# Kernel optimization log

Hardware: AMD Instinct MI355X
Metric: run time of the kernel (lower is better)

## Reference

```python
import jax, jax.numpy as jnp
import numpy as np

N_WORDS_BATCH = 16384   # words in the forward batch
EMB_DIM = 128
NUM_ROOTS = 2048
VOCAB = 65536
BOOST = 1.5             # attention_boost_factor
EPS = 1e-8


def setup_inputs() -> dict:
    key = jax.random.key(0)
    k0, k1, k2, k3, k4 = jax.random.split(key, 5)
    word_indices = jax.random.randint(k0, (N_WORDS_BATCH,), 0, VOCAB, dtype=jnp.int32)
    root_map = jax.random.randint(k1, (VOCAB,), 0, NUM_ROOTS, dtype=jnp.int32)
    attention_weights = jax.random.uniform(k2, (N_WORDS_BATCH,), dtype=jnp.float32)
    # kaiming_uniform-like init scale
    root_embeddings = jax.random.normal(k3, (NUM_ROOTS, EMB_DIM), dtype=jnp.float32) / np.sqrt(EMB_DIM).astype(np.float32)
    morpho_transforms = jax.random.normal(k4, (NUM_ROOTS, EMB_DIM, EMB_DIM), dtype=jnp.float32) / np.sqrt(EMB_DIM).astype(np.float32)
    root_bias = jnp.zeros((NUM_ROOTS, EMB_DIM), dtype=jnp.float32)
    return {
        'root_embeddings': root_embeddings,
        'morpho_transforms': morpho_transforms,
        'root_bias': root_bias,
        'attention_weights': attention_weights,
        'word_indices': word_indices,
        'root_map': root_map,
    }


def reference(root_embeddings, morpho_transforms, root_bias, attention_weights, word_indices, root_map):
    num_roots = root_embeddings.shape[0]
    roots = root_map[word_indices]                      # (N,) extract_roots

    # extract_equivariant_features: root-indexed gather + per-root matvec
    embs = root_embeddings[roots]                       # (N, D)
    mats = morpho_transforms[roots]                     # (N, D, D)
    feats = jnp.einsum('nij,nj->ni', mats, embs) + root_bias[roots]

    # compute_root_invariant: segment mean over same-root words, gathered back
    ones = jnp.ones(roots.shape, feats.dtype)
    counts = jax.ops.segment_sum(ones, roots, num_segments=num_roots)      # (R,)
    sums = jax.ops.segment_sum(feats, roots, num_segments=num_roots)       # (R, D)
    inv = (sums / jnp.maximum(counts, 1.0)[:, None])[roots]                # (N, D)

    # boost_attention: weight i is multiplied by BOOST once per other word sharing its root,
    # i.e. w_i * BOOST**(count[root_i] - 1), then softmax(log(w + eps)) over the batch.
    c = counts[roots] - 1.0
    boosted = attention_weights * jnp.power(jnp.float32(BOOST), c)
    boosted = jax.nn.softmax(jnp.log(boosted + EPS))

    return inv * boosted[:, None]
```

## Files before the change

kernel.cpp:

```cpp
#include <hip/hip_runtime.h>

#define N_WORDS 16384
#define EMB 128
#define NROOTS 2048
#define EPS 1e-8f
#define LOG2_BOOST 0.5849625007211562f


__global__ void k_roots_hist(const int* __restrict__ wi, const int* __restrict__ rmap,
                             int* __restrict__ roots, int* __restrict__ counts) {
    int n = blockIdx.x * blockDim.x + threadIdx.x;
    int r = rmap[wi[n]];
    roots[n] = r;
    atomicAdd(&counts[r], 1);
}

__global__ void k_matvec(const float* __restrict__ M, const float* __restrict__ e,
                         const float* __restrict__ b, float* __restrict__ g) {
    int r   = blockIdx.x >> 5;
    int row = ((blockIdx.x & 31) << 2) + (threadIdx.x >> 6);
    int lane = threadIdx.x & 63;
    const float2* mrow = (const float2*)(M + ((size_t)r * EMB + row) * EMB);
    const float2* ev   = (const float2*)(e + (size_t)r * EMB);
    float2 m  = mrow[lane];
    float2 ee = ev[lane];
    float acc = m.x * ee.x + m.y * ee.y;
#pragma unroll
    for (int off = 32; off; off >>= 1) acc += __shfl_xor(acc, off, 64);
    if (lane == 0) g[r * EMB + row] = acc + b[r * EMB + row];
}

__global__ void k_boost_sum(const float* __restrict__ w, const int* __restrict__ roots,
                            const int* __restrict__ counts, float* __restrict__ x,
                            float* __restrict__ denom) {
    __shared__ float sred[4];
    int n = blockIdx.x * blockDim.x + threadIdx.x;
    float c = (float)(counts[roots[n]] - 1);
    float v = w[n] * exp2f(c * LOG2_BOOST) + EPS;
    x[n] = v;
#pragma unroll
    for (int off = 32; off; off >>= 1) v += __shfl_xor(v, off, 64);
    int wave = threadIdx.x >> 6, lane = threadIdx.x & 63;
    if (lane == 0) sred[wave] = v;
    __syncthreads();
    if (threadIdx.x == 0) atomicAdd(denom, sred[0] + sred[1] + sred[2] + sred[3]);
}

__global__ void k_out(const float* __restrict__ g, const int* __restrict__ roots,
                      const float* __restrict__ x, const float* __restrict__ denom,
                      float4* __restrict__ out) {
    int idx = blockIdx.x * blockDim.x + threadIdx.x;
    int n = idx >> 5;
    float s = x[n] / *denom;
    const float4* gp = (const float4*)(g + ((size_t)roots[n] << 7));
    float4 v = gp[idx & 31];
    v.x *= s; v.y *= s; v.z *= s; v.w *= s;
    out[idx] = v;
}

extern "C" void kernel_launch(void* const* d_in, const int* in_sizes, int n_in,
                              void* d_out, int out_size, void* d_ws, size_t ws_size,
                              hipStream_t stream) {
    const float* emb  = (const float*)d_in[0];
    const float* M    = (const float*)d_in[1];
    const float* bias = (const float*)d_in[2];
    const float* attw = (const float*)d_in[3];
    const int*   wi   = (const int*)d_in[4];
    const int*   rmap = (const int*)d_in[5];
    float* out = (float*)d_out;

    char* ws = (char*)d_ws;
    int*   counts = (int*)(ws);
    float* denom  = (float*)(ws + 8192);
    int*   roots  = (int*)(ws + 16384);
    float* x      = (float*)(ws + 81920);
    float* g      = (float*)(ws + 147456);

    hipMemsetAsync(ws, 0, 8196, stream);
    k_roots_hist<<<N_WORDS / 256, 256, 0, stream>>>(wi, rmap, roots, counts);
    k_matvec<<<NROOTS * 32, 256, 0, stream>>>(M, emb, bias, g);
    k_boost_sum<<<N_WORDS / 256, 256, 0, stream>>>(attw, roots, counts, x, denom);
    k_out<<<N_WORDS * 32 / 256, 256, 0, stream>>>(g, roots, x, denom, (float4*)out);
}
```

Before: 232.7 us.

## Fuse histogram into matvec launch, widen matvec loads, replace atomic softmax denominator

Merges the root histogram kernel into the matvec launch as extra tail blocks, which removes one kernel launch. The matvec now uses float4 loads with half-wave rows, so each block covers 8 rows and needs half as many blocks. The softmax denominator is written as 64 per-block partials instead of one atomic, and the output kernel reduces those partials itself and recomputes the boosted weight, so the x buffer is gone. The cost is redundant recomputation of the denominator sum and the exp2 in every output thread.

Measured after the change: 207.2 us. 1.12x faster.

```diff
diff --git a/kernel.cpp b/kernel.cpp
--- a/kernel.cpp
+++ b/kernel.cpp
@@ -6,56 +6,65 @@
 #define EPS 1e-8f
 #define LOG2_BOOST 0.5849625007211562f
 
+#define MV_BLOCKS 32768
 
-__global__ void k_roots_hist(const int* __restrict__ wi, const int* __restrict__ rmap,
-                             int* __restrict__ roots, int* __restrict__ counts) {
-    int n = blockIdx.x * blockDim.x + threadIdx.x;
-    int r = rmap[wi[n]];
-    roots[n] = r;
-    atomicAdd(&counts[r], 1);
+
+__global__ void k_fused(const float* __restrict__ M, const float* __restrict__ e,
+                        const float* __restrict__ bias, float* __restrict__ g,
+                        const int* __restrict__ wi, const int* __restrict__ rmap,
+                        int* __restrict__ roots, int* __restrict__ counts) {
+    if (blockIdx.x >= MV_BLOCKS) {
+        int n = (blockIdx.x - MV_BLOCKS) * 256 + threadIdx.x;
+        int r = rmap[wi[n]];
+        roots[n] = r;
+        atomicAdd(&counts[r], 1);
+        return;
+    }
+    int b = blockIdx.x;
+    int r = b >> 4;
+    int wave = threadIdx.x >> 6;
+    int lane = threadIdx.x & 63;
+    int row = ((b & 15) << 3) + (wave << 1) + (lane >> 5);
+    int col = (lane & 31) << 2;
+    size_t rbase = (size_t)r << 7;
+    const float4 m  = *(const float4*)(M + (rbase + row) * EMB + col);
+    const float4 ee = *(const float4*)(e + rbase + col);
+    float acc = fmaf(m.x, ee.x, fmaf(m.y, ee.y, fmaf(m.z, ee.z, m.w * ee.w)));
+#pragma unroll
+    for (int off = 16; off; off >>= 1) acc += __shfl_xor(acc, off, 64);
+    if ((lane & 31) == 0) g[rbase + row] = acc + bias[rbase + row];
 }
 
-__global__ void k_matvec(const float* __restrict__ M, const float* __restrict__ e,
-                         const float* __restrict__ b, float* __restrict__ g) {
-    int r   = blockIdx.x >> 5;
-    int row = ((blockIdx.x & 31) << 2) + (threadIdx.x >> 6);
-    int lane = threadIdx.x & 63;
-    const float2* mrow = (const float2*)(M + ((size_t)r * EMB + row) * EMB);
-    const float2* ev   = (const float2*)(e + (size_t)r * EMB);
-    float2 m  = mrow[lane];
-    float2 ee = ev[lane];
-    float acc = m.x * ee.x + m.y * ee.y;
-#pragma unroll
-    for (int off = 32; off; off >>= 1) acc += __shfl_xor(acc, off, 64);
-    if (lane == 0) g[r * EMB + row] = acc + b[r * EMB + row];
-}
-
-__global__ void k_boost_sum(const float* __restrict__ w, const int* __restrict__ roots,
-                            const int* __restrict__ counts, float* __restrict__ x,
-                            float* __restrict__ denom) {
+__global__ void k_partial(const float* __restrict__ w, const int* __restrict__ roots,
+                          const int* __restrict__ counts, float* __restrict__ partials) {
     __shared__ float sred[4];
-    int n = blockIdx.x * blockDim.x + threadIdx.x;
+    int n = blockIdx.x * 256 + threadIdx.x;
     float c = (float)(counts[roots[n]] - 1);
-    float v = w[n] * exp2f(c * LOG2_BOOST) + EPS;
-    x[n] = v;
+    float v = fmaf(w[n], exp2f(c * LOG2_BOOST), EPS);
 #pragma unroll
     for (int off = 32; off; off >>= 1) v += __shfl_xor(v, off, 64);
     int wave = threadIdx.x >> 6, lane = threadIdx.x & 63;
     if (lane == 0) sred[wave] = v;
     __syncthreads();
-    if (threadIdx.x == 0) atomicAdd(denom, sred[0] + sred[1] + sred[2] + sred[3]);
+    if (threadIdx.x == 0) partials[blockIdx.x] = sred[0] + sred[1] + sred[2] + sred[3];
 }
 
 __global__ void k_out(const float* __restrict__ g, const int* __restrict__ roots,
-                      const float* __restrict__ x, const float* __restrict__ denom,
-                      float4* __restrict__ out) {
-    int idx = blockIdx.x * blockDim.x + threadIdx.x;
+                      const int* __restrict__ counts, const float* __restrict__ w,
+                      const float* __restrict__ partials, float4* __restrict__ out) {
+    int lane = threadIdx.x & 63;
+    float d = partials[lane];
+#pragma unroll
+    for (int off = 32; off; off >>= 1) d += __shfl_xor(d, off, 64);
+    int idx = blockIdx.x * 256 + threadIdx.x;
     int n = idx >> 5;
-    float s = x[n] / *denom;
-    const float4* gp = (const float4*)(g + ((size_t)roots[n] << 7));
-    float4 v = gp[idx & 31];
-    v.x *= s; v.y *= s; v.z *= s; v.w *= s;
-    out[idx] = v;
+    int r = roots[n];
+    float c = (float)(counts[r] - 1);
+    float v = fmaf(w[n], exp2f(c * LOG2_BOOST), EPS);
+    float s = v / d;
+    float4 gv = ((const float4*)(g + ((size_t)r << 7)))[idx & 31];
+    gv.x *= s; gv.y *= s; gv.z *= s; gv.w *= s;
+    out[idx] = gv;
 }
 
 extern "C" void kernel_launch(void* const* d_in, const int* in_sizes, int n_in,
@@ -70,15 +79,13 @@
     float* out = (float*)d_out;
 
     char* ws = (char*)d_ws;
-    int*   counts = (int*)(ws);
-    float* denom  = (float*)(ws + 8192);
-    int*   roots  = (int*)(ws + 16384);
-    float* x      = (float*)(ws + 81920);
-    float* g      = (float*)(ws + 147456);
+    int*   counts   = (int*)(ws);
+    int*   roots    = (int*)(ws + 8192);
+    float* partials = (float*)(ws + 73728);
+    float* g        = (float*)(ws + 73984);
 
-    hipMemsetAsync(ws, 0, 8196, stream);
-    k_roots_hist<<<N_WORDS / 256, 256, 0, stream>>>(wi, rmap, roots, counts);
-    k_matvec<<<NROOTS * 32, 256, 0, stream>>>(M, emb, bias, g);
-    k_boost_sum<<<N_WORDS / 256, 256, 0, stream>>>(attw, roots, counts, x, denom);
-    k_out<<<N_WORDS * 32 / 256, 256, 0, stream>>>(g, roots, x, denom, (float4*)out);
+    hipMemsetAsync(counts, 0, NROOTS * sizeof(int), stream);
+    k_fused<<<MV_BLOCKS + N_WORDS / 256, 256, 0, stream>>>(M, emb, bias, g, wi, rmap, roots, counts);
+    k_partial<<<N_WORDS / 256, 256, 0, stream>>>(attw, roots, counts, partials);
+    k_out<<<N_WORDS * (EMB / 4) / 256, 256, 0, stream>>>(g, roots, counts, attw, partials, (float4*)out);
 }
```
